# Performance work log

Hardware: AMD Instinct MI355X
Metric: run time of the kernel (lower is better)

Reference implementation:

```python
import jax, jax.numpy as jnp
import numpy as np

L, B, E, H, T, V = 256, 64, 256, 256, 16, 50000  # H = per-direction hidden; hidden_dim = 2H


def setup_inputs() -> dict:
    key = jax.random.key(0)
    ks = jax.random.split(key, 32)
    lengths = jnp.sort(jax.random.randint(ks[0], (B,), L // 2, L + 1))[::-1]  # descending, as pack_padded requires
    tokens = jax.random.randint(ks[1], (L, B), 1, V)
    valid = jnp.arange(L)[:, None] < lengths[None, :]
    tokens = jnp.where(valid, tokens, 0)  # pad_index = 0

    def gp(k, shape, s=0.1):
        return jax.random.normal(k, shape, dtype=jnp.float32) * s

    inp = {"tokens": tokens, "lengths": lengths, "emb": gp(ks[2], (V, E))}
    i = 3
    for layer, din in [(0, E), (1, 2 * H)]:
        for d in ("f", "b"):
            inp["w_ih_l%d%s" % (layer, d)] = gp(ks[i], (4 * H, din)); i += 1
            inp["w_hh_l%d%s" % (layer, d)] = gp(ks[i], (4 * H, H)); i += 1
            inp["b_ih_l%d%s" % (layer, d)] = gp(ks[i], (4 * H,)); i += 1
            inp["b_hh_l%d%s" % (layer, d)] = gp(ks[i], (4 * H,)); i += 1
    inp["w_out"] = gp(ks[i], (T, 2 * H)); i += 1
    inp["b_out"] = gp(ks[i], (T,)); i += 1
    inp["start_trans"] = gp(ks[i], (T,)); i += 1
    inp["end_trans"] = gp(ks[i], (T,)); i += 1
    inp["trans"] = gp(ks[i], (T, T))
    return inp


def lstm_layer(x, w_ih, w_hh, b_ih, b_hh):
    # x: [L, B, Din]; PyTorch gate order i, f, g, o; zero init state
    Hd = w_hh.shape[1]
    h0 = jnp.zeros((x.shape[1], Hd), x.dtype)

    def step(carry, xt):
        h, c = carry
        g = xt @ w_ih.T + b_ih + h @ w_hh.T + b_hh
        i, f, gg, o = jnp.split(g, 4, axis=-1)
        c = jax.nn.sigmoid(f) * c + jax.nn.sigmoid(i) * jnp.tanh(gg)
        h = jax.nn.sigmoid(o) * jnp.tanh(c)
        return (h, c), h

    _, ys = jax.lax.scan(step, (h0, h0), x)
    return ys  # [L, B, H]


def reverse_padded(x, lengths):
    # per-sequence time reversal over the first `length` steps (packed-sequence semantics)
    Ls = x.shape[0]
    t = jnp.arange(Ls)[:, None]
    idx = jnp.where(t < lengths[None, :], lengths[None, :] - 1 - t, t)  # [L, B]
    return jnp.take_along_axis(x, idx[:, :, None], axis=0)


def viterbi(emissions, mask, start_trans, end_trans, trans):
    # emissions [L, B, T], mask [L, B] bool -- pytorch-crf Viterbi decode, vectorized over batch
    score0 = start_trans[None, :] + emissions[0]  # [B, T]

    def step(score, inp):
        em_t, m_t = inp  # [B, T], [B]
        nxt = score[:, :, None] + trans[None, :, :] + em_t[:, None, :]  # [B, T, T]
        best = nxt.max(axis=1)
        idx = nxt.argmax(axis=1)  # index of previous tag
        score = jnp.where(m_t[:, None], best, score)  # freeze past end-of-sequence
        return score, idx

    score, hist = jax.lax.scan(step, score0, (emissions[1:], mask[1:]))  # hist [L-1, B, T]
    score = score + end_trans[None, :]
    best_score = score.max(axis=-1)
    last_tag = score.argmax(axis=-1)  # [B]

    def back(cur, inp):
        h_t, m_t = inp
        prev = jnp.take_along_axis(h_t, cur[:, None], axis=1)[:, 0]
        cur = jnp.where(m_t, prev, cur)
        return cur, cur

    _, tags_head = jax.lax.scan(back, last_tag, (hist, mask[1:]), reverse=True)  # [L-1, B]
    tags = jnp.concatenate([tags_head, last_tag[None, :]], axis=0)  # [L, B]
    tags = jnp.where(mask, tags, 0)
    return best_score, tags.astype(jnp.int32)


def reference(tokens, lengths, emb,
              w_ih_l0f, w_hh_l0f, b_ih_l0f, b_hh_l0f,
              w_ih_l0b, w_hh_l0b, b_ih_l0b, b_hh_l0b,
              w_ih_l1f, w_hh_l1f, b_ih_l1f, b_hh_l1f,
              w_ih_l1b, w_hh_l1b, b_ih_l1b, b_hh_l1b,
              w_out, b_out, start_trans, end_trans, trans):
    mask = tokens != 0  # pad_index = 0
    x = emb[tokens]  # [L, B, E]
    layers = [((w_ih_l0f, w_hh_l0f, b_ih_l0f, b_hh_l0f), (w_ih_l0b, w_hh_l0b, b_ih_l0b, b_hh_l0b)),
              ((w_ih_l1f, w_hh_l1f, b_ih_l1f, b_hh_l1f), (w_ih_l1b, w_hh_l1b, b_ih_l1b, b_hh_l1b))]
    for pf, pb in layers:
        fwd = lstm_layer(x, *pf)
        bwd = reverse_padded(lstm_layer(reverse_padded(x, lengths), *pb), lengths)
        x = jnp.concatenate([fwd, bwd], axis=-1) * mask[:, :, None]  # zero pads like pad_packed_sequence
    emissions = x @ w_out.T + b_out  # [L, B, T]
    best_score, tags = viterbi(emissions, mask, start_trans, end_trans, trans)
    return best_score, tags
```

## Files before the change

### kernel.cpp

```cpp
#include <hip/hip_runtime.h>
#include <hip/hip_bf16.h>
#include <math.h>

#define LSEQ 256
#define BB   64
#define EE   256

__global__ __launch_bounds__(64)
void embed_kernel(const int* __restrict__ tokens, const float* __restrict__ emb,
                  float* __restrict__ x0) {
    int r = blockIdx.x;
    int tok = tokens[r];
    const float4* src = (const float4*)(emb + (size_t)tok * EE);
    float4* dst = (float4*)(x0 + (size_t)r * EE);
    dst[threadIdx.x] = src[threadIdx.x];
}

__global__ __launch_bounds__(256)
void pack_w3_kernel(const float* __restrict__ w0, const float* __restrict__ w1,
                    const float* __restrict__ w2, const float* __restrict__ w3,
                    float* __restrict__ W3) {
    __shared__ float t[16][65];
    const float* w = blockIdx.z == 0 ? w0 : blockIdx.z == 1 ? w1 : blockIdx.z == 2 ? w2 : w3;
    float* out = W3 + (size_t)blockIdx.z * 262144;
    int ut = blockIdx.y;
    int g = blockIdx.x >> 2, kt = blockIdx.x & 3;
    int k0 = kt * 64, tid = threadIdx.x;
    for (int e = tid; e < 1024; e += 256) {
        int ul = e >> 6, kl = e & 63;
        t[ul][kl] = w[(size_t)(g * 256 + ut * 16 + ul) * 256 + k0 + kl];
    }
    __syncthreads();
    for (int e = tid; e < 1024; e += 256) {
        int kl = e >> 4, ul = e & 15;
        out[(size_t)(ut * 256 + k0 + kl) * 64 + g * 16 + ul] = t[ul][kl];
    }
}

__global__ __launch_bounds__(256)
void init_flags_kernel(int* __restrict__ flags) {
    flags[blockIdx.x * 256 + threadIdx.x] = 0;
}

__global__ __launch_bounds__(256)
void gemm_bias_kernel(const float* __restrict__ A, const float* __restrict__ W,
                      const float* __restrict__ b1, const float* __restrict__ b2,
                      float* __restrict__ C, int M, int N, int K) {
    const int BK = 16;
    __shared__ float As[BK][128];
    __shared__ float Bs[BK][128];
    int tid = threadIdx.x;
    int bm = blockIdx.x * 128;
    int bn = blockIdx.y * 128;
    int tm = (tid >> 4) << 3;
    int tn = (tid & 15) << 3;
    int lr = tid >> 1;
    int lc = (tid & 1) << 3;
    const float* Ap = A + (size_t)(bm + lr) * K + lc;
    const float* Wpt = W + (size_t)(bn + lr) * K + lc;
    float acc[8][8];
#pragma unroll
    for (int i = 0; i < 8; i++)
#pragma unroll
        for (int j = 0; j < 8; j++) acc[i][j] = 0.f;

    for (int k0 = 0; k0 < K; k0 += BK) {
        float4 a0 = *(const float4*)(Ap + k0);
        float4 a1 = *(const float4*)(Ap + k0 + 4);
        float4 w0 = *(const float4*)(Wpt + k0);
        float4 w1 = *(const float4*)(Wpt + k0 + 4);
        __syncthreads();
        As[lc+0][lr]=a0.x; As[lc+1][lr]=a0.y; As[lc+2][lr]=a0.z; As[lc+3][lr]=a0.w;
        As[lc+4][lr]=a1.x; As[lc+5][lr]=a1.y; As[lc+6][lr]=a1.z; As[lc+7][lr]=a1.w;
        Bs[lc+0][lr]=w0.x; Bs[lc+1][lr]=w0.y; Bs[lc+2][lr]=w0.z; Bs[lc+3][lr]=w0.w;
        Bs[lc+4][lr]=w1.x; Bs[lc+5][lr]=w1.y; Bs[lc+6][lr]=w1.z; Bs[lc+7][lr]=w1.w;
        __syncthreads();
#pragma unroll
        for (int k = 0; k < BK; k++) {
            float av[8], bv[8];
            *(float4*)&av[0] = *(const float4*)&As[k][tm];
            *(float4*)&av[4] = *(const float4*)&As[k][tm+4];
            *(float4*)&bv[0] = *(const float4*)&Bs[k][tn];
            *(float4*)&bv[4] = *(const float4*)&Bs[k][tn+4];
#pragma unroll
            for (int i = 0; i < 8; i++)
#pragma unroll
                for (int j = 0; j < 8; j++) acc[i][j] = fmaf(av[i], bv[j], acc[i][j]);
        }
    }
    float bj[8];
#pragma unroll
    for (int j = 0; j < 8; j++) bj[j] = b1[bn+tn+j] + b2[bn+tn+j];
#pragma unroll
    for (int i = 0; i < 8; i++) {
        float4 v0, v1;
        v0.x = acc[i][0]+bj[0]; v0.y = acc[i][1]+bj[1]; v0.z = acc[i][2]+bj[2]; v0.w = acc[i][3]+bj[3];
        v1.x = acc[i][4]+bj[4]; v1.y = acc[i][5]+bj[5]; v1.z = acc[i][6]+bj[6]; v1.w = acc[i][7]+bj[7];
        *(float4*)&C[(size_t)(bm+tm+i)*N + bn+tn]     = v0;
        *(float4*)&C[(size_t)(bm+tm+i)*N + bn+tn + 4] = v1;
    }
}

template<bool AX>
__device__ __forceinline__ void scan_body(int tk,
        const float* __restrict__ G_f, const float* __restrict__ G_b,
        const float* __restrict__ W3f, const float* __restrict__ W3b,
        const int* __restrict__ lengths, float* __restrict__ xout,
        float* __restrict__ hg, int* __restrict__ flags, float* smem) {
    float* hs = smem;
    float* P  = smem + 2048;
    const int dom = tk & 15;
    const int ut  = tk >> 4;
    const int dir = dom & 1;
    const int bt  = dom >> 1;
    const float* __restrict__ G = dir ? G_b : G_f;
    const float* __restrict__ W3 = (dir ? W3b : W3f) + (size_t)ut * 16384;
    float* hgD = hg + (size_t)dom * 4096;
    int* flgD  = flags + dom * 512;

    const int tid = threadIdx.x;
    const int kg = tid >> 5, cw = tid & 31;
    const int w  = tid >> 6, lane = tid & 63;
    const int cb = (tid >> 4) & 7, cu = tid & 15;
    const int bg = bt * 8 + cb;
    const int ug = ut * 16 + cu;
    const int mylen = lengths[bg];

    float2 wreg[32];
#pragma unroll
    for (int kk = 0; kk < 32; kk++)
        wreg[kk] = *(const float2*)&W3[(size_t)(kg * 32 + kk) * 64 + cw * 2];

#pragma unroll
    for (int i = 0; i < 8; i++) hs[tid + 256 * i] = 0.f;

    float cstate = 0.f;
    int tcur = dir ? (mylen - 1) : 0;
    float gp0 = 0.f, gp1 = 0.f, gp2 = 0.f, gp3 = 0.f;
    if (tid < 128) {
        const float* gr = G + ((size_t)(tcur * BB + bg)) * 1024 + ug;
        gp0 = gr[0]; gp1 = gr[256]; gp2 = gr[512]; gp3 = gr[768];
    }
    __syncthreads();

    for (int s = 0; s < LSEQ; s++) {
        if (s > 0) {
            if (lane < 4) {
                const int* fp = &flgD[(4 * w + lane) * 32];
                while (__hip_atomic_load(fp, __ATOMIC_RELAXED, __HIP_MEMORY_SCOPE_AGENT) < s)
                    __builtin_amdgcn_s_sleep(1);
            }
            asm volatile("" ::: "memory");
            const unsigned long long* src =
                (const unsigned long long*)(hgD + ((s - 1) & 1) * 2048) + w * 256;
            unsigned long long v[4];
#pragma unroll
            for (int i = 0; i < 4; i++)
                v[i] = __hip_atomic_load(src + lane + 64 * i, __ATOMIC_RELAXED,
                                         __HIP_MEMORY_SCOPE_AGENT);
#pragma unroll
            for (int i = 0; i < 4; i++) {
                int fo = 512 * w + 2 * (lane + 64 * i);
                hs[fo]     = __uint_as_float((unsigned)v[i]);
                hs[fo + 1] = __uint_as_float((unsigned)(v[i] >> 32));
            }
            asm volatile("" ::: "memory");
        }

        float2 acc[8];
        const float4* h4 = (const float4*)hs;
#pragma unroll
        for (int b = 0; b < 8; b++) {
            float2 a = make_float2(0.f, 0.f);
            int hb0 = 64 * kg + 4 * b;
#pragma unroll
            for (int q = 0; q < 4; q++) {
                float4 hv = h4[hb0 + q];
                float2 w0 = wreg[q*4+0], w1 = wreg[q*4+1], w2 = wreg[q*4+2], w3v = wreg[q*4+3];
                a.x = fmaf(w0.x, hv.x, a.x); a.y = fmaf(w0.y, hv.x, a.y);
                a.x = fmaf(w1.x, hv.y, a.x); a.y = fmaf(w1.y, hv.y, a.y);
                a.x = fmaf(w2.x, hv.z, a.x); a.y = fmaf(w2.y, hv.z, a.y);
                a.x = fmaf(w3v.x, hv.w, a.x); a.y = fmaf(w3v.y, hv.w, a.y);
            }
#pragma unroll
            for (int q = 0; q < 4; q++) {
                float4 hv = h4[hb0 + 32 + q];
                float2 w0 = wreg[16+q*4+0], w1 = wreg[16+q*4+1], w2 = wreg[16+q*4+2], w3v = wreg[16+q*4+3];
                a.x = fmaf(w0.x, hv.x, a.x); a.y = fmaf(w0.y, hv.x, a.y);
                a.x = fmaf(w1.x, hv.y, a.x); a.y = fmaf(w1.y, hv.y, a.y);
                a.x = fmaf(w2.x, hv.z, a.x); a.y = fmaf(w2.y, hv.z, a.y);
                a.x = fmaf(w3v.x, hv.w, a.x); a.y = fmaf(w3v.y, hv.w, a.y);
            }
            acc[b] = a;
        }
        const int wofs = (cw * 2) ^ (kg * 2);
#pragma unroll
        for (int b = 0; b < 8; b++)
            *(float2*)&P[kg * 512 + b * 64 + wofs] = acc[b];
        __syncthreads();

        float xv = 0.f;
        size_t xr = 0;
        if (tid < 128) {
            float a0 = gp0, a1 = gp1, a2 = gp2, a3 = gp3;
#pragma unroll
            for (int k2 = 0; k2 < 8; k2++) {
                int base = k2 * 512 + cb * 64, x = k2 * 2;
                a0 += P[base + ((cu)      ^ x)];
                a1 += P[base + ((16 + cu) ^ x)];
                a2 += P[base + ((32 + cu) ^ x)];
                a3 += P[base + ((48 + cu) ^ x)];
            }
            float iv = 1.f / (1.f + expf(-a0));
            float fv = 1.f / (1.f + expf(-a1));
            float gv = tanhf(a2);
            float ov = 1.f / (1.f + expf(-a3));
            cstate = fv * cstate + iv * gv;
            float h = ov * tanhf(cstate);
            float hp = __shfl_xor(h, 1);
            if (!(cu & 1)) {
                unsigned long long pv =
                    ((unsigned long long)__float_as_uint(hp) << 32) | __float_as_uint(h);
                atomicExch((unsigned long long*)&hgD[(s & 1) * 2048 + ut * 128 + cb * 16 + cu], pv);
            }
            xv = (s < mylen) ? h : 0.f;
            xr = (size_t)(tcur * BB + bg) * 512 + dir * 256 + ug;
            if (AX) {
                float xp = __shfl_xor(xv, 1);
                if (!(cu & 1)) {
                    unsigned long long pv2 =
                        ((unsigned long long)__float_as_uint(xp) << 32) | __float_as_uint(xv);
                    atomicExch((unsigned long long*)&xout[xr], pv2);
                }
            }
        }
        asm volatile("s_waitcnt vmcnt(0)" ::: "memory");
        __syncthreads();
        if (tid == 0) atomicExch(&flgD[ut * 32], s + 1);
        if (tid < 128) {
            if (!AX) xout[xr] = xv;
            if (s < LSEQ - 1) {
                int s2 = s + 1;
                tcur = dir ? (s2 < mylen ? mylen - 1 - s2 : s2) : s2;
                const float* gr = G + ((size_t)(tcur * BB + bg)) * 1024 + ug;
                gp0 = gr[0]; gp1 = gr[256]; gp2 = gr[512]; gp3 = gr[768];
            }
        }
    }
}

__global__ __launch_bounds__(256, 1)
void mega1_kernel(const float* __restrict__ G0f, const float* __restrict__ G0b,
                  const float* __restrict__ W30f, const float* __restrict__ W30b,
                  const int* __restrict__ lengths, float* __restrict__ x1,
                  float* __restrict__ hg, int* __restrict__ flags,
                  const float* __restrict__ w1f, const float* __restrict__ b1f_ih,
                  const float* __restrict__ b1f_hh,
                  const float* __restrict__ w1b, const float* __restrict__ b1b_ih,
                  const float* __restrict__ b1b_hh,
                  float* __restrict__ G1f, float* __restrict__ G1b,
                  int* __restrict__ ticket) {
    __shared__ float smem[6144];
    __shared__ int sTk;
    if (threadIdx.x == 0) sTk = atomicAdd(ticket, 1);
    __syncthreads();
    const int tk = sTk;

    if (tk < 256) {
        scan_body<true>(tk, G0f, G0b, W30f, W30b, lengths, x1, hg, flags, smem);
        return;
    }

    const int gb = tk - 256;
    const int mb_r = gb >> 4;
    const int mb = (mb_r & 1) ? (63 - (mb_r >> 1)) : (64 + (mb_r >> 1));
    const int nb = gb & 15;
    const int tid = threadIdx.x;

    {
        int domD = tid >> 4, utf = tid & 15;
        int dirD = domD & 1, btD = domD >> 1;
        int t1 = mb * 2 + 1;
        int req = t1;
        if (dirD) {
            req = 0;
            for (int i = 0; i < 8; i++) {
                int len = lengths[btD * 8 + i];
                int t0 = t1 - 1;
                int w0 = t0 < len ? len - 1 - t0 : t0;
                int w1 = t1 < len ? len - 1 - t1 : t1;
                int wv = w0 > w1 ? w0 : w1;
                if (wv > req) req = wv;
            }
        }
        const int* fp = flags + domD * 512 + utf * 32;
        while (__hip_atomic_load(fp, __ATOMIC_RELAXED, __HIP_MEMORY_SCOPE_AGENT) < req + 1)
            __builtin_amdgcn_s_sleep(32);
    }
    __syncthreads();

    const float* Wm; const float* bb1; const float* bb2; float* Cout; int bn;
    if (nb < 8) { Wm = w1f; bb1 = b1f_ih; bb2 = b1f_hh; Cout = G1f; bn = nb * 128; }
    else        { Wm = w1b; bb1 = b1b_ih; bb2 = b1b_hh; Cout = G1b; bn = (nb - 8) * 128; }

    float* As = smem;
    float* Bs = smem + 2048;
    const int bm = mb * 128;
    const int tm = (tid >> 4) << 3;
    const int tn = (tid & 15) << 3;
    const int lr = tid >> 1;
    const int lc = (tid & 1) << 3;
    const float* Ap = x1 + (size_t)(bm + lr) * 512 + lc;
    const float* Wpt = Wm + (size_t)(bn + lr) * 512 + lc;
    float acc[8][8];
#pragma unroll
    for (int i = 0; i < 8; i++)
#pragma unroll
        for (int j = 0; j < 8; j++) acc[i][j] = 0.f;

    for (int k0 = 0; k0 < 512; k0 += 16) {
        float4 a0 = *(const float4*)(Ap + k0);
        float4 a1 = *(const float4*)(Ap + k0 + 4);
        float4 w0 = *(const float4*)(Wpt + k0);
        float4 w1 = *(const float4*)(Wpt + k0 + 4);
        __syncthreads();
        As[(lc+0)*128+lr]=a0.x; As[(lc+1)*128+lr]=a0.y; As[(lc+2)*128+lr]=a0.z; As[(lc+3)*128+lr]=a0.w;
        As[(lc+4)*128+lr]=a1.x; As[(lc+5)*128+lr]=a1.y; As[(lc+6)*128+lr]=a1.z; As[(lc+7)*128+lr]=a1.w;
        Bs[(lc+0)*128+lr]=w0.x; Bs[(lc+1)*128+lr]=w0.y; Bs[(lc+2)*128+lr]=w0.z; Bs[(lc+3)*128+lr]=w0.w;
        Bs[(lc+4)*128+lr]=w1.x; Bs[(lc+5)*128+lr]=w1.y; Bs[(lc+6)*128+lr]=w1.z; Bs[(lc+7)*128+lr]=w1.w;
        __syncthreads();
#pragma unroll
        for (int k = 0; k < 16; k++) {
            float av[8], bv[8];
            *(float4*)&av[0] = *(const float4*)&As[k*128+tm];
            *(float4*)&av[4] = *(const float4*)&As[k*128+tm+4];
            *(float4*)&bv[0] = *(const float4*)&Bs[k*128+tn];
            *(float4*)&bv[4] = *(const float4*)&Bs[k*128+tn+4];
#pragma unroll
            for (int i = 0; i < 8; i++)
#pragma unroll
                for (int j = 0; j < 8; j++) acc[i][j] = fmaf(av[i], bv[j], acc[i][j]);
        }
    }
    float bj[8];
#pragma unroll
    for (int j = 0; j < 8; j++) bj[j] = bb1[bn+tn+j] + bb2[bn+tn+j];
#pragma unroll
    for (int i = 0; i < 8; i++) {
        float4 v0, v1;
        v0.x = acc[i][0]+bj[0]; v0.y = acc[i][1]+bj[1]; v0.z = acc[i][2]+bj[2]; v0.w = acc[i][3]+bj[3];
        v1.x = acc[i][4]+bj[4]; v1.y = acc[i][5]+bj[5]; v1.z = acc[i][6]+bj[6]; v1.w = acc[i][7]+bj[7];
        *(float4*)&Cout[(size_t)(bm+tm+i)*1024 + bn+tn]     = v0;
        *(float4*)&Cout[(size_t)(bm+tm+i)*1024 + bn+tn + 4] = v1;
    }
}

__global__ __launch_bounds__(256, 1)
void scan1_kernel(const float* __restrict__ G_f, const float* __restrict__ G_b,
                  const float* __restrict__ W3f, const float* __restrict__ W3b,
                  const int* __restrict__ lengths, float* __restrict__ xout,
                  float* __restrict__ hg, int* __restrict__ flags) {
    __shared__ float smem[6144];
    scan_body<false>(blockIdx.x, G_f, G_b, W3f, W3b, lengths, xout, hg, flags, smem);
}

__global__ __launch_bounds__(256)
void emis_kernel(const float* __restrict__ x, const float* __restrict__ w_out,
                 const float* __restrict__ b_out, float* __restrict__ em) {
    __shared__ float ws_[16][516];
    __shared__ float xs[16][516];
    int tid = threadIdx.x;
    size_t r0 = (size_t)blockIdx.x * 16;
    for (int i4 = tid; i4 < 2048; i4 += 256) {
        int r = i4 >> 7, k4 = (i4 & 127) << 2;
        *(float4*)&ws_[r][k4] = *(const float4*)&w_out[r*512 + k4];
        *(float4*)&xs[r][k4]  = *(const float4*)&x[(r0 + r)*512 + k4];
    }
    __syncthreads();
    int rr = tid >> 4, n = tid & 15;
    const float4* xr = (const float4*)&xs[rr][0];
    const float4* wr = (const float4*)&ws_[n][0];
    float4 s; s.x = s.y = s.z = s.w = 0.f;
#pragma unroll 8
    for (int k = 0; k < 128; k++) {
        float4 a = xr[k], b = wr[k];
        s.x = fmaf(a.x,b.x,s.x); s.y = fmaf(a.y,b.y,s.y);
        s.z = fmaf(a.z,b.z,s.z); s.w = fmaf(a.w,b.w,s.w);
    }
    em[(r0+rr)*16 + n] = s.x+s.y+s.z+s.w + b_out[n];
}

__global__ __launch_bounds__(64)
void viterbi_kernel(const float* __restrict__ em, const int* __restrict__ tokens,
                    const float* __restrict__ start_trans, const float* __restrict__ end_trans,
                    const float* __restrict__ trans, float* __restrict__ out) {
    __shared__ float em_s[256][16];
    __shared__ float tr_s[16][16];
    __shared__ float sc[16];
    __shared__ unsigned char hist[255][16];
    int b = blockIdx.x, tid = threadIdx.x;
    for (int i = tid; i < 4096; i += 64) {
        int t = i >> 4, n = i & 15;
        em_s[t][n] = em[(size_t)t*1024 + b*16 + n];
    }
    for (int i = tid; i < 256; i += 64) ((float*)tr_s)[i] = trans[i];
    __syncthreads();
    if (tid < 16) sc[tid] = start_trans[tid] + em_s[0][tid];
    __syncthreads();
    for (int t = 1; t < 256; t++) {
        float best = 0.f; int arg = 0;
        if (tid < 16) {
            best = sc[0] + tr_s[0][tid];
#pragma unroll
            for (int i = 1; i < 16; i++) {
                float v = sc[i] + tr_s[i][tid];
                if (v > best) { best = v; arg = i; }
            }
            best += em_s[t][tid];
            hist[t-1][tid] = (unsigned char)arg;
        }
        bool m = tokens[t*64 + b] != 0;
        __syncthreads();
        if (tid < 16 && m) sc[tid] = best;
        __syncthreads();
    }
    if (tid == 0) {
        float best = sc[0] + end_trans[0]; int cur = 0;
        for (int jj = 1; jj < 16; jj++) {
            float v = sc[jj] + end_trans[jj];
            if (v > best) { best = v; cur = jj; }
        }
        out[b] = best;
        float* tags = out + 64;
        tags[255*64 + b] = (tokens[255*64+b] != 0) ? (float)cur : 0.f;
        for (int t = 254; t >= 0; t--) {
            if (tokens[(t+1)*64 + b] != 0) cur = hist[t][cur];
            tags[t*64 + b] = (tokens[t*64+b] != 0) ? (float)cur : 0.f;
        }
    }
}

extern "C" void kernel_launch(void* const* d_in, const int* in_sizes, int n_in,
                              void* d_out, int out_size, void* d_ws, size_t ws_size,
                              hipStream_t stream) {
    const int*   tokens   = (const int*)d_in[0];
    const int*   lengths  = (const int*)d_in[1];
    const float* emb      = (const float*)d_in[2];
    const float* w_ih_l0f = (const float*)d_in[3];
    const float* w_hh_l0f = (const float*)d_in[4];
    const float* b_ih_l0f = (const float*)d_in[5];
    const float* b_hh_l0f = (const float*)d_in[6];
    const float* w_ih_l0b = (const float*)d_in[7];
    const float* w_hh_l0b = (const float*)d_in[8];
    const float* b_ih_l0b = (const float*)d_in[9];
    const float* b_hh_l0b = (const float*)d_in[10];
    const float* w_ih_l1f = (const float*)d_in[11];
    const float* w_hh_l1f = (const float*)d_in[12];
    const float* b_ih_l1f = (const float*)d_in[13];
    const float* b_hh_l1f = (const float*)d_in[14];
    const float* w_ih_l1b = (const float*)d_in[15];
    const float* w_hh_l1b = (const float*)d_in[16];
    const float* b_ih_l1b = (const float*)d_in[17];
    const float* b_hh_l1b = (const float*)d_in[18];
    const float* w_out    = (const float*)d_in[19];
    const float* b_out    = (const float*)d_in[20];
    const float* start_tr = (const float*)d_in[21];
    const float* end_tr   = (const float*)d_in[22];
    const float* trans    = (const float*)d_in[23];

    float* ws   = (float*)d_ws;
    float* x0   = ws;
    float* x12  = x0 + 4194304;
    float* Gf   = x12 + 8388608;
    float* Gb   = Gf + 16777216;
    float* W3   = Gb + 16777216;
    float* W30f = W3, *W30b = W3 + 262144, *W31f = W3 + 524288, *W31b = W3 + 786432;
    float* hg   = W3 + 1048576;
    int*   flags  = (int*)(hg + 65536);
    int*   ticket = flags + 16384;
    float* em   = x0;

    embed_kernel<<<16384, 64, 0, stream>>>(tokens, emb, x0);
    pack_w3_kernel<<<dim3(16, 16, 4), 256, 0, stream>>>(w_hh_l0f, w_hh_l0b, w_hh_l1f, w_hh_l1b, W3);
    init_flags_kernel<<<65, 256, 0, stream>>>(flags);

    dim3 gg(128, 8);
    gemm_bias_kernel<<<gg, 256, 0, stream>>>(x0, w_ih_l0f, b_ih_l0f, b_hh_l0f, Gf, 16384, 1024, 256);
    gemm_bias_kernel<<<gg, 256, 0, stream>>>(x0, w_ih_l0b, b_ih_l0b, b_hh_l0b, Gb, 16384, 1024, 256);

    mega1_kernel<<<2304, 256, 0, stream>>>(Gf, Gb, W30f, W30b, lengths, x12, hg, flags,
                                           w_ih_l1f, b_ih_l1f, b_hh_l1f,
                                           w_ih_l1b, b_ih_l1b, b_hh_l1b,
                                           Gf, Gb, ticket);

    scan1_kernel<<<256, 256, 0, stream>>>(Gf, Gb, W31f, W31b, lengths, x12, hg, flags + 8192);

    emis_kernel<<<1024, 256, 0, stream>>>(x12, w_out, b_out, em);
    viterbi_kernel<<<64, 64, 0, stream>>>(em, tokens, start_tr, end_tr, trans, (float*)d_out);
}
```

Baseline: 2.564 ms.

## Use global step counter for GEMM waits, prefetch GEMM tiles, widen embed blocks

The fused layer-1 GEMM blocks no longer poll 256 per-domain flags with all threads. A single thread now waits on one global per-step counter that every scan block increments. Both GEMM loops prefetch the next K-tile into registers before computing on the current one, and the embedding gather handles four rows per 256-thread block. The aim is less polling traffic, hidden global load latency and fewer tiny blocks. The cost is an extra atomic per scan step and a coarser dependency: GEMM blocks now wait for the worst case over all 64 sequences.

```diff
diff --git a/kernel.cpp b/kernel.cpp
--- a/kernel.cpp
+++ b/kernel.cpp
@@ -6,14 +6,14 @@
 #define BB   64
 #define EE   256
 
-__global__ __launch_bounds__(64)
+__global__ __launch_bounds__(256)
 void embed_kernel(const int* __restrict__ tokens, const float* __restrict__ emb,
                   float* __restrict__ x0) {
-    int r = blockIdx.x;
+    int r = blockIdx.x * 4 + (threadIdx.x >> 6);
+    int lane4 = threadIdx.x & 63;
     int tok = tokens[r];
-    const float4* src = (const float4*)(emb + (size_t)tok * EE);
-    float4* dst = (float4*)(x0 + (size_t)r * EE);
-    dst[threadIdx.x] = src[threadIdx.x];
+    ((float4*)(x0 + (size_t)r * EE))[lane4] =
+        ((const float4*)(emb + (size_t)tok * EE))[lane4];
 }
 
 __global__ __launch_bounds__(256)
@@ -64,17 +64,26 @@
 #pragma unroll
         for (int j = 0; j < 8; j++) acc[i][j] = 0.f;
 
-    for (int k0 = 0; k0 < K; k0 += BK) {
-        float4 a0 = *(const float4*)(Ap + k0);
-        float4 a1 = *(const float4*)(Ap + k0 + 4);
-        float4 w0 = *(const float4*)(Wpt + k0);
-        float4 w1 = *(const float4*)(Wpt + k0 + 4);
+    float4 a0 = *(const float4*)(Ap);
+    float4 a1 = *(const float4*)(Ap + 4);
+    float4 w0 = *(const float4*)(Wpt);
+    float4 w1 = *(const float4*)(Wpt + 4);
+
+    const int nIt = K >> 4;
+    for (int it = 0; it < nIt; it++) {
         __syncthreads();
         As[lc+0][lr]=a0.x; As[lc+1][lr]=a0.y; As[lc+2][lr]=a0.z; As[lc+3][lr]=a0.w;
         As[lc+4][lr]=a1.x; As[lc+5][lr]=a1.y; As[lc+6][lr]=a1.z; As[lc+7][lr]=a1.w;
         Bs[lc+0][lr]=w0.x; Bs[lc+1][lr]=w0.y; Bs[lc+2][lr]=w0.z; Bs[lc+3][lr]=w0.w;
         Bs[lc+4][lr]=w1.x; Bs[lc+5][lr]=w1.y; Bs[lc+6][lr]=w1.z; Bs[lc+7][lr]=w1.w;
         __syncthreads();
+        if (it + 1 < nIt) {
+            const int k0 = (it + 1) << 4;
+            a0 = *(const float4*)(Ap + k0);
+            a1 = *(const float4*)(Ap + k0 + 4);
+            w0 = *(const float4*)(Wpt + k0);
+            w1 = *(const float4*)(Wpt + k0 + 4);
+        }
 #pragma unroll
         for (int k = 0; k < BK; k++) {
             float av[8], bv[8];
@@ -106,7 +115,8 @@
         const float* __restrict__ G_f, const float* __restrict__ G_b,
         const float* __restrict__ W3f, const float* __restrict__ W3b,
         const int* __restrict__ lengths, float* __restrict__ xout,
-        float* __restrict__ hg, int* __restrict__ flags, float* smem) {
+        float* __restrict__ hg, int* __restrict__ flags, int* __restrict__ cnt,
+        float* smem) {
     float* hs = smem;
     float* P  = smem + 2048;
     const int dom = tk & 15;
@@ -237,6 +247,7 @@
         asm volatile("s_waitcnt vmcnt(0)" ::: "memory");
         __syncthreads();
         if (tid == 0) atomicExch(&flgD[ut * 32], s + 1);
+        if (cnt != nullptr && tid == 64) atomicAdd(&cnt[s * 32], 1);
         if (tid < 128) {
             if (!AX) xout[xr] = xv;
             if (s < LSEQ - 1) {
@@ -253,7 +264,7 @@
 void mega1_kernel(const float* __restrict__ G0f, const float* __restrict__ G0b,
                   const float* __restrict__ W30f, const float* __restrict__ W30b,
                   const int* __restrict__ lengths, float* __restrict__ x1,
-                  float* __restrict__ hg, int* __restrict__ flags,
+                  float* __restrict__ hg, int* __restrict__ flags, int* __restrict__ cnt,
                   const float* __restrict__ w1f, const float* __restrict__ b1f_ih,
                   const float* __restrict__ b1f_hh,
                   const float* __restrict__ w1b, const float* __restrict__ b1b_ih,
@@ -267,7 +278,7 @@
     const int tk = sTk;
 
     if (tk < 256) {
-        scan_body<true>(tk, G0f, G0b, W30f, W30b, lengths, x1, hg, flags, smem);
+        scan_body<true>(tk, G0f, G0b, W30f, W30b, lengths, x1, hg, flags, cnt, smem);
         return;
     }
 
@@ -277,25 +288,20 @@
     const int nb = gb & 15;
     const int tid = threadIdx.x;
 
-    {
-        int domD = tid >> 4, utf = tid & 15;
-        int dirD = domD & 1, btD = domD >> 1;
+    if (tid == 0) {
         int t1 = mb * 2 + 1;
         int req = t1;
-        if (dirD) {
-            req = 0;
-            for (int i = 0; i < 8; i++) {
-                int len = lengths[btD * 8 + i];
-                int t0 = t1 - 1;
-                int w0 = t0 < len ? len - 1 - t0 : t0;
-                int w1 = t1 < len ? len - 1 - t1 : t1;
-                int wv = w0 > w1 ? w0 : w1;
-                if (wv > req) req = wv;
-            }
-        }
-        const int* fp = flags + domD * 512 + utf * 32;
-        while (__hip_atomic_load(fp, __ATOMIC_RELAXED, __HIP_MEMORY_SCOPE_AGENT) < req + 1)
-            __builtin_amdgcn_s_sleep(32);
+        for (int i = 0; i < 64; i++) {
+            int len = lengths[i];
+            int t0 = t1 - 1;
+            int w0 = t0 < len ? len - 1 - t0 : t0;
+            int w1 = t1 < len ? len - 1 - t1 : t1;
+            int wv = w0 > w1 ? w0 : w1;
+            if (wv > req) req = wv;
+        }
+        const int* cp = &cnt[req * 32];
+        while (__hip_atomic_load(cp, __ATOMIC_RELAXED, __HIP_MEMORY_SCOPE_AGENT) < 256)
+            __builtin_amdgcn_s_sleep(64);
     }
     __syncthreads();
 
@@ -318,17 +324,25 @@
 #pragma unroll
         for (int j = 0; j < 8; j++) acc[i][j] = 0.f;
 
-    for (int k0 = 0; k0 < 512; k0 += 16) {
-        float4 a0 = *(const float4*)(Ap + k0);
-        float4 a1 = *(const float4*)(Ap + k0 + 4);
-        float4 w0 = *(const float4*)(Wpt + k0);
-        float4 w1 = *(const float4*)(Wpt + k0 + 4);
+    float4 a0 = *(const float4*)(Ap);
+    float4 a1 = *(const float4*)(Ap + 4);
+    float4 w0 = *(const float4*)(Wpt);
+    float4 w1 = *(const float4*)(Wpt + 4);
+
+    for (int it = 0; it < 32; it++) {
         __syncthreads();
         As[(lc+0)*128+lr]=a0.x; As[(lc+1)*128+lr]=a0.y; As[(lc+2)*128+lr]=a0.z; As[(lc+3)*128+lr]=a0.w;
         As[(lc+4)*128+lr]=a1.x; As[(lc+5)*128+lr]=a1.y; As[(lc+6)*128+lr]=a1.z; As[(lc+7)*128+lr]=a1.w;
         Bs[(lc+0)*128+lr]=w0.x; Bs[(lc+1)*128+lr]=w0.y; Bs[(lc+2)*128+lr]=w0.z; Bs[(lc+3)*128+lr]=w0.w;
         Bs[(lc+4)*128+lr]=w1.x; Bs[(lc+5)*128+lr]=w1.y; Bs[(lc+6)*128+lr]=w1.z; Bs[(lc+7)*128+lr]=w1.w;
         __syncthreads();
+        if (it + 1 < 32) {
+            const int k0 = (it + 1) << 4;
+            a0 = *(const float4*)(Ap + k0);
+            a1 = *(const float4*)(Ap + k0 + 4);
+            w0 = *(const float4*)(Wpt + k0);
+            w1 = *(const float4*)(Wpt + k0 + 4);
+        }
 #pragma unroll
         for (int k = 0; k < 16; k++) {
             float av[8], bv[8];
@@ -361,7 +375,7 @@
                   const int* __restrict__ lengths, float* __restrict__ xout,
                   float* __restrict__ hg, int* __restrict__ flags) {
     __shared__ float smem[6144];
-    scan_body<false>(blockIdx.x, G_f, G_b, W3f, W3b, lengths, xout, hg, flags, smem);
+    scan_body<false>(blockIdx.x, G_f, G_b, W3f, W3b, lengths, xout, hg, flags, nullptr, smem);
 }
 
 __global__ __launch_bounds__(256)
@@ -477,18 +491,19 @@
     float* W30f = W3, *W30b = W3 + 262144, *W31f = W3 + 524288, *W31b = W3 + 786432;
     float* hg   = W3 + 1048576;
     int*   flags  = (int*)(hg + 65536);
-    int*   ticket = flags + 16384;
+    int*   cnt    = flags + 16384;
+    int*   ticket = cnt + 8192;
     float* em   = x0;
 
-    embed_kernel<<<16384, 64, 0, stream>>>(tokens, emb, x0);
+    embed_kernel<<<4096, 256, 0, stream>>>(tokens, emb, x0);
     pack_w3_kernel<<<dim3(16, 16, 4), 256, 0, stream>>>(w_hh_l0f, w_hh_l0b, w_hh_l1f, w_hh_l1b, W3);
-    init_flags_kernel<<<65, 256, 0, stream>>>(flags);
+    init_flags_kernel<<<97, 256, 0, stream>>>(flags);
 
     dim3 gg(128, 8);
     gemm_bias_kernel<<<gg, 256, 0, stream>>>(x0, w_ih_l0f, b_ih_l0f, b_hh_l0f, Gf, 16384, 1024, 256);
     gemm_bias_kernel<<<gg, 256, 0, stream>>>(x0, w_ih_l0b, b_ih_l0b, b_hh_l0b, Gb, 16384, 1024, 256);
 
-    mega1_kernel<<<2304, 256, 0, stream>>>(Gf, Gb, W30f, W30b, lengths, x12, hg, flags,
+    mega1_kernel<<<2304, 256, 0, stream>>>(Gf, Gb, W30f, W30b, lengths, x12, hg, flags, cnt,
                                            w_ih_l1f, b_ih_l1f, b_hh_l1f,
                                            w_ih_l1b, b_ih_l1b, b_hh_l1b,
                                            Gf, Gb, ticket);
```

New measurement: 2.503 ms. 2.4% less time.
